# Kernel optimization log

Measured on AMD Instinct MI355X. Metric: run time of the kernel, lower is better.

The kernel has to match this reference:

```python
import jax, jax.numpy as jnp
import numpy as np

D_MODEL = 1024
NHEAD = 16
D_K = D_MODEL // NHEAD


def setup_inputs() -> dict:
    key = jax.random.key(0)
    ks = jax.random.split(key, 12)
    B, S = 1, 4096
    s = 1.0 / np.sqrt(D_MODEL)
    inp = {
        "query": jax.random.normal(ks[0], (B, S, D_MODEL), jnp.float32),
        "key": jax.random.normal(ks[1], (B, S, D_MODEL), jnp.float32),
        "value": jax.random.normal(ks[2], (B, S, D_MODEL), jnp.float32),
        "W_q": jax.random.normal(ks[3], (D_MODEL, D_MODEL), jnp.float32) * s,
        "b_q": jnp.zeros((D_MODEL,), jnp.float32),
        "W_k": jax.random.normal(ks[4], (D_MODEL, D_MODEL), jnp.float32) * s,
        "b_k": jnp.zeros((D_MODEL,), jnp.float32),
        "W_v": jax.random.normal(ks[5], (D_MODEL, D_MODEL), jnp.float32) * s,
        "b_v": jnp.zeros((D_MODEL,), jnp.float32),
        "W_o": jax.random.normal(ks[6], (D_MODEL, D_MODEL), jnp.float32) * s,
        "b_o": jnp.zeros((D_MODEL,), jnp.float32),
    }
    return inp


def reference(query, key, value, W_q, b_q, W_k, b_k, W_v, b_v, W_o, b_o):
    B, S, _ = query.shape
    # linear projections (torch Linear: x @ W.T + b)
    Q = query @ W_q.T + b_q
    K = key @ W_k.T + b_k
    V = value @ W_v.T + b_v
    # split heads: [B, S, D] -> [B, H, S, d_k]
    Q = Q.reshape(B, S, NHEAD, D_K).transpose(0, 2, 1, 3)
    K = K.reshape(B, S, NHEAD, D_K).transpose(0, 2, 1, 3)
    V = V.reshape(B, S, NHEAD, D_K).transpose(0, 2, 1, 3)
    # scaled dot-product attention (materializes [B,H,S,S] like original)
    scores = jnp.einsum("bhqd,bhkd->bhqk", Q, K) / jnp.sqrt(jnp.float32(D_K))
    weights = jax.nn.softmax(scores, axis=-1)
    attn = jnp.einsum("bhqk,bhkd->bhqd", weights, V)
    # combine heads: [B, H, S, d_k] -> [B, S, D]
    attn = attn.transpose(0, 2, 1, 3).reshape(B, S, D_MODEL)
    return attn @ W_o.T + b_o
```

## Files before the change

kernel.cpp:

```cpp
#include <hip/hip_runtime.h>
#include <hip/hip_bf16.h>
#include <type_traits>

constexpr int SEQ = 4096;
constexpr int DMODEL = 1024;
constexpr int NH = 16;
constexpr int DKH = 64;
constexpr float SCALE = 0.125f;
constexpr float SCALE2 = 0.125f * 1.4426950408889634f;

typedef __bf16 bf16x8 __attribute__((ext_vector_type(8)));
typedef __bf16 bf16x4 __attribute__((ext_vector_type(4)));
typedef float f32x4 __attribute__((ext_vector_type(4)));
typedef float f32x16 __attribute__((ext_vector_type(16)));
typedef unsigned int u32x4 __attribute__((ext_vector_type(4)));
union W8 { u32x4 u; bf16x8 v; };

__device__ inline void store_c(__hip_bfloat16* p, float v) { *p = __float2bfloat16(v); }
__device__ inline void store_c(float* p, float v) { *p = v; }

typedef const void __attribute__((address_space(1)))* gas_ptr;
typedef void __attribute__((address_space(3)))* las_ptr;
__device__ inline void load_lds_16B(const void* g, void* l) {
  __builtin_amdgcn_global_load_lds((gas_ptr)g, (las_ptr)l, 16, 0, 0);
}

__device__ inline unsigned pack2(float a, float b) {
  union { __bf16 h[2]; unsigned u; } p;
  p.h[0] = (__bf16)a; p.h[1] = (__bf16)b;
  return p.u;
}

__device__ inline void st8(__hip_bfloat16* buf, int row, int col, bf16x8 v) {
  *(bf16x8*)(buf + row * 64 + (col ^ ((row & 7) << 3))) = v;
}
__device__ inline bf16x8 ld8(const __hip_bfloat16* buf, int row, int col) {
  return *(const bf16x8*)(buf + row * 64 + (col ^ ((row & 7) << 3)));
}

__global__ __launch_bounds__(256)
void cvt_all(const float* __restrict__ q, const float* __restrict__ k,
             const float* __restrict__ v, const float* __restrict__ wq,
             const float* __restrict__ wk, const float* __restrict__ wv,
             const float* __restrict__ wo,
             __bf16* __restrict__ Xq, __bf16* __restrict__ Xk,
             __bf16* __restrict__ Xv, __bf16* __restrict__ Wqb,
             __bf16* __restrict__ Wkb, __bf16* __restrict__ Wvb,
             __bf16* __restrict__ Wob) {
  const int b = blockIdx.x;
  const float* src; __bf16* dst; size_t base;
  if      (b < 2048) { src = q;  dst = Xq;  base = b; }
  else if (b < 4096) { src = k;  dst = Xk;  base = b - 2048; }
  else if (b < 6144) { src = v;  dst = Xv;  base = b - 4096; }
  else if (b < 6656) { src = wq; dst = Wqb; base = b - 6144; }
  else if (b < 7168) { src = wk; dst = Wkb; base = b - 6656; }
  else if (b < 7680) { src = wv; dst = Wvb; base = b - 7168; }
  else               { src = wo; dst = Wob; base = b - 7680; }
  const size_t i = (base * 256 + threadIdx.x) * 8;
  const float4 a = *(const float4*)(src + i);
  const float4 c = *(const float4*)(src + i + 4);
  bf16x8 r = {(__bf16)a.x, (__bf16)a.y, (__bf16)a.z, (__bf16)a.w,
              (__bf16)c.x, (__bf16)c.y, (__bf16)c.z, (__bf16)c.w};
  *(bf16x8*)(dst + i) = r;
}

constexpr int BK = 64;

template <typename TC, bool TRANS_C>
__global__ __launch_bounds__(256)
void gemm_bf16_lds(const __bf16* __restrict__ A,
                   const __bf16* __restrict__ W,
                   const float* __restrict__ bias,
                   TC* __restrict__ C,
                   float out_scale) {
  __shared__ alignas(16) __bf16 As[64][64];
  __shared__ alignas(16) __bf16 Ws[64][64];

  const int t = threadIdx.x;
  const int lane = t & 63;
  const int w = t >> 6;
  const int wr = w >> 1;
  const int wc = w & 1;
  const int col = lane & 15;
  const int quad = lane >> 4;
  const int m_blk = blockIdx.y * 64;
  const int n_blk = blockIdx.x * 64;

  const int srow = t >> 3;
  const int scol = (t & 7) * 8;

  f32x4 acc[2][2] = {};

  for (int k0 = 0; k0 < DMODEL; k0 += BK) {
    __syncthreads();
    #pragma unroll
    for (int p = 0; p < 2; ++p)
      load_lds_16B(A + (size_t)(m_blk + p * 32 + srow) * DMODEL + k0 + scol,
                   &As[p * 32 + srow][scol]);
    #pragma unroll
    for (int p = 0; p < 2; ++p)
      load_lds_16B(W + (size_t)(n_blk + p * 32 + srow) * DMODEL + k0 + scol,
                   &Ws[p * 32 + srow][scol]);
    __syncthreads();

    #pragma unroll
    for (int kh = 0; kh < BK; kh += 32) {
      bf16x8 af[2], bfr[2];
      #pragma unroll
      for (int at = 0; at < 2; ++at)
        af[at] = *(const bf16x8*)&As[wr * 32 + at * 16 + col][kh + quad * 8];
      #pragma unroll
      for (int bt = 0; bt < 2; ++bt)
        bfr[bt] = *(const bf16x8*)&Ws[wc * 32 + bt * 16 + col][kh + quad * 8];
      #pragma unroll
      for (int at = 0; at < 2; ++at)
        #pragma unroll
        for (int bt = 0; bt < 2; ++bt)
          acc[at][bt] = __builtin_amdgcn_mfma_f32_16x16x32_bf16(
              af[at], bfr[bt], acc[at][bt], 0, 0, 0);
    }
  }

  #pragma unroll
  for (int at = 0; at < 2; ++at) {
    #pragma unroll
    for (int bt = 0; bt < 2; ++bt) {
      const int n = n_blk + wc * 32 + bt * 16 + col;
      const float b = bias[n];
      #pragma unroll
      for (int i = 0; i < 4; ++i) {
        const int m = m_blk + wr * 32 + at * 16 + quad * 4 + i;
        const float v = (acc[at][bt][i] + b) * out_scale;
        if constexpr (TRANS_C) store_c(&C[(size_t)n * SEQ + m], v);
        else                   store_c(&C[(size_t)m * DMODEL + n], v);
      }
    }
  }
}

constexpr int LDK = 72;

template <typename TA, typename TC, bool TRANS_C>
__global__ __launch_bounds__(256)
void gemm_tiled(const TA* __restrict__ A,
                const float* __restrict__ W,
                const float* __restrict__ bias,
                TC* __restrict__ C,
                float out_scale) {
  __shared__ alignas(16) __bf16 As[128][LDK];
  __shared__ alignas(16) __bf16 Ws[64][LDK];

  const int t = threadIdx.x;
  const int lane = t & 63;
  const int w = t >> 6;
  const int wr = w >> 1;
  const int wc = w & 1;
  const int col = lane & 15;
  const int quad = lane >> 4;
  const int m_blk = blockIdx.y * 128;
  const int n_blk = blockIdx.x * 64;

  f32x4 acc[4][2] = {};

  for (int k0 = 0; k0 < DMODEL; k0 += BK) {
    __syncthreads();
    if constexpr (std::is_same<TA, float>::value) {
      #pragma unroll
      for (int p = 0; p < 8; ++p) {
        const int r = p * 16 + (t >> 4);
        const int c = (t & 15) * 4;
        const float4 v =
            *(const float4*)(A + (size_t)(m_blk + r) * DMODEL + k0 + c);
        bf16x4 b = {(__bf16)v.x, (__bf16)v.y, (__bf16)v.z, (__bf16)v.w};
        *(bf16x4*)&As[r][c] = b;
      }
    } else {
      #pragma unroll
      for (int p = 0; p < 4; ++p) {
        const int r = p * 32 + (t >> 3);
        const int c = (t & 7) * 8;
        *(bf16x8*)&As[r][c] =
            *(const bf16x8*)((const __bf16*)A + (size_t)(m_blk + r) * DMODEL + k0 + c);
      }
    }
    #pragma unroll
    for (int p = 0; p < 4; ++p) {
      const int r = p * 16 + (t >> 4);
      const int c = (t & 15) * 4;
      const float4 v =
          *(const float4*)(W + (size_t)(n_blk + r) * DMODEL + k0 + c);
      bf16x4 b = {(__bf16)v.x, (__bf16)v.y, (__bf16)v.z, (__bf16)v.w};
      *(bf16x4*)&Ws[r][c] = b;
    }
    __syncthreads();

    #pragma unroll
    for (int kh = 0; kh < BK; kh += 32) {
      bf16x8 af[4], bfr[2];
      #pragma unroll
      for (int at = 0; at < 4; ++at)
        af[at] = *(const bf16x8*)&As[wr * 64 + at * 16 + col][kh + quad * 8];
      #pragma unroll
      for (int bt = 0; bt < 2; ++bt)
        bfr[bt] = *(const bf16x8*)&Ws[wc * 32 + bt * 16 + col][kh + quad * 8];
      #pragma unroll
      for (int at = 0; at < 4; ++at)
        #pragma unroll
        for (int bt = 0; bt < 2; ++bt)
          acc[at][bt] = __builtin_amdgcn_mfma_f32_16x16x32_bf16(
              af[at], bfr[bt], acc[at][bt], 0, 0, 0);
    }
  }

  #pragma unroll
  for (int at = 0; at < 4; ++at) {
    #pragma unroll
    for (int bt = 0; bt < 2; ++bt) {
      const int n = n_blk + wc * 32 + bt * 16 + col;
      const float b = bias[n];
      #pragma unroll
      for (int i = 0; i < 4; ++i) {
        const int m = m_blk + wr * 64 + at * 16 + quad * 4 + i;
        const float v = (acc[at][bt][i] + b) * out_scale;
        if constexpr (TRANS_C) store_c(&C[(size_t)n * SEQ + m], v);
        else                   store_c(&C[(size_t)m * DMODEL + n], v);
      }
    }
  }
}

__global__ __launch_bounds__(256, 4)
void flash_attn_split32(const __hip_bfloat16* __restrict__ Q,
                        const __hip_bfloat16* __restrict__ K,
                        const __hip_bfloat16* __restrict__ Vt,
                        __hip_bfloat16* __restrict__ Opart,
                        float* __restrict__ lsum_g) {
  __shared__ alignas(16) __hip_bfloat16 kt[64 * 64];
  __shared__ alignas(16) __hip_bfloat16 vtt[64 * 64];

  const int t = threadIdx.x;
  const int lane = t & 63;
  const int w = t >> 6;
  const int head = blockIdx.y;
  const int q0 = blockIdx.x * 128;
  const int z = blockIdx.z;
  const int l31 = lane & 31;
  const int hl = lane >> 5;

  bf16x8 qf[4];
  {
    const __hip_bfloat16* qp =
        Q + (size_t)(q0 + w * 32 + l31) * DMODEL + head * DKH + hl * 8;
    #pragma unroll
    for (int db = 0; db < 4; ++db) qf[db] = *(const bf16x8*)(qp + db * 16);
  }

  f32x16 acc_o[2] = {};
  float lsa = 0.f, lsb = 0.f;

  const int sr = t >> 2;
  const int sc = (t & 3) * 16;
  const int kbeg = z * (SEQ / 2);
  constexpr int NT = (SEQ / 2) / 64;

  const __hip_bfloat16* kgp = K + (size_t)(kbeg + sr) * DMODEL + head * DKH + sc;
  const __hip_bfloat16* vgp = Vt + (size_t)(head * DKH + sr) * SEQ + kbeg + sc;

  bf16x8 kr0 = *(const bf16x8*)kgp;
  bf16x8 kr1 = *(const bf16x8*)(kgp + 8);
  bf16x8 vr0 = *(const bf16x8*)vgp;
  bf16x8 vr1 = *(const bf16x8*)(vgp + 8);

  for (int ti = 0; ti < NT; ++ti) {
    __syncthreads();
    st8(kt, sr, sc, kr0);  st8(kt, sr, sc + 8, kr1);
    st8(vtt, sr, sc, vr0); st8(vtt, sr, sc + 8, vr1);
    __syncthreads();

    if (ti + 1 < NT) {
      const __hip_bfloat16* kn = kgp + (size_t)(ti + 1) * 64 * DMODEL;
      const __hip_bfloat16* vn = vgp + (ti + 1) * 64;
      kr0 = *(const bf16x8*)kn; kr1 = *(const bf16x8*)(kn + 8);
      vr0 = *(const bf16x8*)vn; vr1 = *(const bf16x8*)(vn + 8);
    }

    bf16x8 pa[4];
    #pragma unroll
    for (int kb = 0; kb < 2; ++kb) {
      f32x16 s = {};
      #pragma unroll
      for (int db = 0; db < 4; ++db) {
        const bf16x8 kf = ld8(kt, kb * 32 + l31, db * 16 + hl * 8);
        s = __builtin_amdgcn_mfma_f32_32x32x16_bf16(kf, qf[db], s, 0, 0, 0);
      }
      unsigned wp[8];
      #pragma unroll
      for (int i = 0; i < 8; ++i) {
        const float p0 = __builtin_amdgcn_exp2f(s[2 * i]);
        const float p1 = __builtin_amdgcn_exp2f(s[2 * i + 1]);
        lsa += p0; lsb += p1;
        wp[i] = pack2(p0, p1);
      }
      #pragma unroll
      for (int b = 0; b < 2; ++b) {
        const unsigned x0 = (unsigned)__shfl_xor((int)wp[4 * b + 0], 32);
        const unsigned x1 = (unsigned)__shfl_xor((int)wp[4 * b + 1], 32);
        const unsigned x2 = (unsigned)__shfl_xor((int)wp[4 * b + 2], 32);
        const unsigned x3 = (unsigned)__shfl_xor((int)wp[4 * b + 3], 32);
        W8 u;
        u.u[0] = hl ? x2 : wp[4 * b + 0];
        u.u[1] = hl ? x3 : wp[4 * b + 1];
        u.u[2] = hl ? wp[4 * b + 2] : x0;
        u.u[3] = hl ? wp[4 * b + 3] : x1;
        pa[kb * 2 + b] = u.v;
      }
    }

    #pragma unroll
    for (int db = 0; db < 2; ++db)
      #pragma unroll
      for (int kq = 0; kq < 4; ++kq) {
        const bf16x8 vb = ld8(vtt, db * 32 + l31, kq * 16 + hl * 8);
        acc_o[db] = __builtin_amdgcn_mfma_f32_32x32x16_bf16(
            pa[kq], vb, acc_o[db], 0, 0, 0);
      }
  }

  float lsumq = lsa + lsb;
  lsumq += __shfl_xor(lsumq, 32);
  if (lane < 32)
    lsum_g[((size_t)z * NH + head) * SEQ + q0 + w * 32 + lane] = lsumq;

  __hip_bfloat16* O = Opart + (size_t)z * SEQ * DMODEL;
  #pragma unroll
  for (int db = 0; db < 2; ++db)
    #pragma unroll
    for (int r = 0; r < 16; ++r) {
      const int qr = q0 + w * 32 + (r & 3) + 8 * (r >> 2) + 4 * hl;
      const int c = head * DKH + db * 32 + l31;
      O[(size_t)qr * DMODEL + c] = __float2bfloat16(acc_o[db][r]);
    }
}

__global__ __launch_bounds__(256)
void attn_combine(const __hip_bfloat16* __restrict__ Op,
                  const float* __restrict__ ls,
                  __hip_bfloat16* __restrict__ Ao) {
  const size_t i = ((size_t)blockIdx.x * 256 + threadIdx.x) * 8;
  const int qrow = (int)(i >> 10);
  const int h = (int)((i & 1023) >> 6);
  const float inv = 1.f / (ls[(size_t)h * SEQ + qrow] +
                           ls[(size_t)(NH + h) * SEQ + qrow]);
  const bf16x8 a = *(const bf16x8*)(Op + i);
  const bf16x8 b = *(const bf16x8*)(Op + (size_t)SEQ * DMODEL + i);
  bf16x8 r;
  #pragma unroll
  for (int j = 0; j < 8; ++j)
    r[j] = (__bf16)(((float)a[j] + (float)b[j]) * inv);
  *(bf16x8*)(Ao + i) = r;
}

constexpr int LDP = 72;
constexpr float SHIFT = 8.0f;

__global__ __launch_bounds__(256)
void flash_attn_mono(const __hip_bfloat16* __restrict__ Q,
                     const __hip_bfloat16* __restrict__ K,
                     const __hip_bfloat16* __restrict__ Vt,
                     __hip_bfloat16* __restrict__ O) {
  __shared__ alignas(16) __hip_bfloat16 kt[64][LDP];
  __shared__ alignas(16) __hip_bfloat16 vtt[DKH][LDP];
  __shared__ alignas(16) __hip_bfloat16 plT[4][32][LDP];

  const int t = threadIdx.x;
  const int lane = t & 63;
  const int w = t >> 6;
  const int h = blockIdx.y;
  const int q0 = blockIdx.x * 128;
  const int col = lane & 15;
  const int quad = lane >> 4;

  bf16x8 qf[2][2];
  #pragma unroll
  for (int rg = 0; rg < 2; ++rg) {
    const __hip_bfloat16* qptr =
        Q + (size_t)(q0 + w * 32 + rg * 16 + col) * DMODEL + h * DKH + quad * 8;
    qf[rg][0] = *(const bf16x8*)qptr;
    qf[rg][1] = *(const bf16x8*)(qptr + 32);
  }

  f32x4 acc_o[2][4] = {};
  float lsumq[2] = {0.f, 0.f};
  const int sr = t >> 2;
  const int sc = (t & 3) * 16;

  for (int k0 = 0; k0 < SEQ; k0 += 64) {
    __syncthreads();
    const __hip_bfloat16* kg = K + (size_t)(k0 + sr) * DMODEL + h * DKH + sc;
    *(bf16x8*)&kt[sr][sc]     = *(const bf16x8*)kg;
    *(bf16x8*)&kt[sr][sc + 8] = *(const bf16x8*)(kg + 8);
    const __hip_bfloat16* vg = Vt + (size_t)(h * DKH + sr) * SEQ + k0 + sc;
    *(bf16x8*)&vtt[sr][sc]     = *(const bf16x8*)vg;
    *(bf16x8*)&vtt[sr][sc + 8] = *(const bf16x8*)(vg + 8);
    __syncthreads();

    #pragma unroll
    for (int jt = 0; jt < 4; ++jt) {
      const bf16x8 kf0 = *(const bf16x8*)&kt[jt * 16 + col][quad * 8];
      const bf16x8 kf1 = *(const bf16x8*)&kt[jt * 16 + col][quad * 8 + 32];
      #pragma unroll
      for (int rg = 0; rg < 2; ++rg) {
        f32x4 zz = {0.f, 0.f, 0.f, 0.f};
        zz = __builtin_amdgcn_mfma_f32_16x16x32_bf16(kf0, qf[rg][0], zz, 0, 0, 0);
        zz = __builtin_amdgcn_mfma_f32_16x16x32_bf16(kf1, qf[rg][1], zz, 0, 0, 0);
        bf16x4 pk;
        #pragma unroll
        for (int r = 0; r < 4; ++r) {
          const float p = __expf(zz[r] - SHIFT);
          lsumq[rg] += p;
          pk[r] = (__bf16)p;
        }
        *(bf16x4*)&plT[w][rg * 16 + col][jt * 16 + quad * 4] = pk;
      }
    }

    bf16x8 pa[2][2];
    #pragma unroll
    for (int rg = 0; rg < 2; ++rg) {
      pa[rg][0] = *(const bf16x8*)&plT[w][rg * 16 + col][quad * 8];
      pa[rg][1] = *(const bf16x8*)&plT[w][rg * 16 + col][quad * 8 + 32];
    }
    #pragma unroll
    for (int jt = 0; jt < 4; ++jt) {
      const bf16x8 vb0 = *(const bf16x8*)&vtt[jt * 16 + col][quad * 8];
      const bf16x8 vb1 = *(const bf16x8*)&vtt[jt * 16 + col][quad * 8 + 32];
      #pragma unroll
      for (int rg = 0; rg < 2; ++rg) {
        acc_o[rg][jt] = __builtin_amdgcn_mfma_f32_16x16x32_bf16(
            pa[rg][0], vb0, acc_o[rg][jt], 0, 0, 0);
        acc_o[rg][jt] = __builtin_amdgcn_mfma_f32_16x16x32_bf16(
            pa[rg][1], vb1, acc_o[rg][jt], 0, 0, 0);
      }
    }
  }

  #pragma unroll
  for (int rg = 0; rg < 2; ++rg) {
    lsumq[rg] += __shfl_xor(lsumq[rg], 16);
    lsumq[rg] += __shfl_xor(lsumq[rg], 32);
  }
  float invr[2][4];
  #pragma unroll
  for (int rg = 0; rg < 2; ++rg)
    #pragma unroll
    for (int r = 0; r < 4; ++r)
      invr[rg][r] = 1.f / __shfl(lsumq[rg], quad * 4 + r);

  #pragma unroll
  for (int rg = 0; rg < 2; ++rg) {
    #pragma unroll
    for (int jt = 0; jt < 4; ++jt) {
      #pragma unroll
      for (int r = 0; r < 4; ++r) {
        const int qr = q0 + w * 32 + rg * 16 + quad * 4 + r;
        const int c = h * DKH + jt * 16 + col;
        O[(size_t)qr * DMODEL + c] = __float2bfloat16(acc_o[rg][jt][r] * invr[rg][r]);
      }
    }
  }
}

extern "C" void kernel_launch(void* const* d_in, const int* in_sizes, int n_in,
                              void* d_out, int out_size, void* d_ws, size_t ws_size,
                              hipStream_t stream) {
  const float* query = (const float*)d_in[0];
  const float* key   = (const float*)d_in[1];
  const float* value = (const float*)d_in[2];
  const float* W_q   = (const float*)d_in[3];
  const float* b_q   = (const float*)d_in[4];
  const float* W_k   = (const float*)d_in[5];
  const float* b_k   = (const float*)d_in[6];
  const float* W_v   = (const float*)d_in[7];
  const float* b_v   = (const float*)d_in[8];
  const float* W_o   = (const float*)d_in[9];
  const float* b_o   = (const float*)d_in[10];

  float* out = (float*)d_out;
  const size_t mat = (size_t)SEQ * DMODEL;
  const size_t MB = 1024 * 1024;

  char* ws = (char*)d_ws;
  __hip_bfloat16* Qp = (__hip_bfloat16*)d_out;
  __hip_bfloat16* Kp = (__hip_bfloat16*)ws;
  __hip_bfloat16* Vt = Kp + mat;

  dim3 gblock(256);
  dim3 ggrid(DMODEL / 64, SEQ / 64);

  if (ws_size >= 40 * MB) {
    __bf16* Xq  = (__bf16*)((char*)d_out + 8 * MB);
    __bf16* Xk  = (__bf16*)(ws + 16 * MB);
    __bf16* Xv  = (__bf16*)(ws + 24 * MB);
    __bf16* Wqb = (__bf16*)(ws + 32 * MB);
    __bf16* Wkb = (__bf16*)(ws + 34 * MB);
    __bf16* Wvb = (__bf16*)(ws + 36 * MB);
    __bf16* Wob = (__bf16*)(ws + 38 * MB);
    __hip_bfloat16* Opart = (__hip_bfloat16*)(ws + 16 * MB);
    float* lsum = (float*)(ws + 32 * MB);
    __hip_bfloat16* Ao = (__hip_bfloat16*)(ws + 16 * MB);

    hipLaunchKernelGGL(cvt_all, dim3(8192), gblock, 0, stream,
                       query, key, value, W_q, W_k, W_v, W_o,
                       Xq, Xk, Xv, Wqb, Wkb, Wvb, Wob);

    hipLaunchKernelGGL((gemm_bf16_lds<__hip_bfloat16, false>), ggrid, gblock,
                       0, stream, Xq, Wqb, b_q, Qp, SCALE2);
    hipLaunchKernelGGL((gemm_bf16_lds<__hip_bfloat16, false>), ggrid, gblock,
                       0, stream, Xk, Wkb, b_k, Kp, 1.0f);
    hipLaunchKernelGGL((gemm_bf16_lds<__hip_bfloat16, true>), ggrid, gblock,
                       0, stream, Xv, Wvb, b_v, Vt, 1.0f);

    dim3 agrid(SEQ / 128, NH, 2);
    hipLaunchKernelGGL(flash_attn_split32, agrid, gblock, 0, stream,
                       Qp, Kp, Vt, Opart, lsum);
    hipLaunchKernelGGL(attn_combine, dim3(2048), gblock, 0, stream,
                       Opart, lsum, Ao);

    hipLaunchKernelGGL((gemm_bf16_lds<float, false>), ggrid, gblock, 0, stream,
                       (const __bf16*)Ao, Wob, b_o, out, 1.0f);
  } else {
    __hip_bfloat16* Ao = Qp + mat;
    float* Cw = (float*)d_ws;
    dim3 fgrid(DMODEL / 64, SEQ / 128);
    hipLaunchKernelGGL((gemm_tiled<float, __hip_bfloat16, false>), fgrid, gblock,
                       0, stream, query, W_q, b_q, Qp, SCALE);
    hipLaunchKernelGGL((gemm_tiled<float, __hip_bfloat16, false>), fgrid, gblock,
                       0, stream, key, W_k, b_k, Kp, 1.0f);
    hipLaunchKernelGGL((gemm_tiled<float, __hip_bfloat16, true>), fgrid, gblock,
                       0, stream, value, W_v, b_v, Vt, 1.0f);
    dim3 agrid(SEQ / 128, NH);
    hipLaunchKernelGGL(flash_attn_mono, agrid, gblock, 0, stream, Qp, Kp, Vt, Ao);
    hipLaunchKernelGGL((gemm_tiled<__hip_bfloat16, float, false>), fgrid, gblock,
                       0, stream, Ao, W_o, b_o, Cw, 1.0f);
    hipMemcpyAsync(out, Cw, mat * sizeof(float), hipMemcpyDeviceToDevice, stream);
  }
}
```

Before: 293.6 us.

## Enlarge GEMM tiles to 128x64, batch QKV projections, tune attention inner loop

The bf16 GEMM now computes 128x64 output tiles per block, so each wave holds 4x2 MFMA accumulators and the A tile is reused across more columns. The three Q/K/V projections run as one launch with a z-dimension that selects the operands, which cuts launch count and fills the GPU with more blocks. In flash attention, the cross-half shuffles are replaced with v_permlane32_swap, and s_setprio raises wave priority around the MFMA sections. The cost is higher register and LDS use per block, which may lower occupancy.

```diff
diff --git a/kernel.cpp b/kernel.cpp
--- a/kernel.cpp
+++ b/kernel.cpp
@@ -68,12 +68,12 @@
 
 template <typename TC, bool TRANS_C>
 __global__ __launch_bounds__(256)
-void gemm_bf16_lds(const __bf16* __restrict__ A,
-                   const __bf16* __restrict__ W,
-                   const float* __restrict__ bias,
-                   TC* __restrict__ C,
-                   float out_scale) {
-  __shared__ alignas(16) __bf16 As[64][64];
+void gemm128(const __bf16* __restrict__ A,
+             const __bf16* __restrict__ W,
+             const float* __restrict__ bias,
+             TC* __restrict__ C,
+             float out_scale) {
+  __shared__ alignas(16) __bf16 As[128][64];
   __shared__ alignas(16) __bf16 Ws[64][64];
 
   const int t = threadIdx.x;
@@ -83,18 +83,18 @@
   const int wc = w & 1;
   const int col = lane & 15;
   const int quad = lane >> 4;
-  const int m_blk = blockIdx.y * 64;
+  const int m_blk = blockIdx.y * 128;
   const int n_blk = blockIdx.x * 64;
 
   const int srow = t >> 3;
   const int scol = (t & 7) * 8;
 
-  f32x4 acc[2][2] = {};
+  f32x4 acc[4][2] = {};
 
   for (int k0 = 0; k0 < DMODEL; k0 += BK) {
     __syncthreads();
     #pragma unroll
-    for (int p = 0; p < 2; ++p)
+    for (int p = 0; p < 4; ++p)
       load_lds_16B(A + (size_t)(m_blk + p * 32 + srow) * DMODEL + k0 + scol,
                    &As[p * 32 + srow][scol]);
     #pragma unroll
@@ -105,15 +105,15 @@
 
     #pragma unroll
     for (int kh = 0; kh < BK; kh += 32) {
-      bf16x8 af[2], bfr[2];
-      #pragma unroll
-      for (int at = 0; at < 2; ++at)
-        af[at] = *(const bf16x8*)&As[wr * 32 + at * 16 + col][kh + quad * 8];
+      bf16x8 af[4], bfr[2];
+      #pragma unroll
+      for (int at = 0; at < 4; ++at)
+        af[at] = *(const bf16x8*)&As[wr * 64 + at * 16 + col][kh + quad * 8];
       #pragma unroll
       for (int bt = 0; bt < 2; ++bt)
         bfr[bt] = *(const bf16x8*)&Ws[wc * 32 + bt * 16 + col][kh + quad * 8];
       #pragma unroll
-      for (int at = 0; at < 2; ++at)
+      for (int at = 0; at < 4; ++at)
         #pragma unroll
         for (int bt = 0; bt < 2; ++bt)
           acc[at][bt] = __builtin_amdgcn_mfma_f32_16x16x32_bf16(
@@ -122,17 +122,97 @@
   }
 
   #pragma unroll
-  for (int at = 0; at < 2; ++at) {
+  for (int at = 0; at < 4; ++at) {
     #pragma unroll
     for (int bt = 0; bt < 2; ++bt) {
       const int n = n_blk + wc * 32 + bt * 16 + col;
       const float b = bias[n];
       #pragma unroll
       for (int i = 0; i < 4; ++i) {
-        const int m = m_blk + wr * 32 + at * 16 + quad * 4 + i;
+        const int m = m_blk + wr * 64 + at * 16 + quad * 4 + i;
         const float v = (acc[at][bt][i] + b) * out_scale;
         if constexpr (TRANS_C) store_c(&C[(size_t)n * SEQ + m], v);
         else                   store_c(&C[(size_t)m * DMODEL + n], v);
+      }
+    }
+  }
+}
+
+__global__ __launch_bounds__(256)
+void gemm_qkv(const __bf16* __restrict__ Xq, const __bf16* __restrict__ Xk,
+              const __bf16* __restrict__ Xv, const __bf16* __restrict__ Wq,
+              const __bf16* __restrict__ Wk, const __bf16* __restrict__ Wv,
+              const float* __restrict__ bq, const float* __restrict__ bk,
+              const float* __restrict__ bv,
+              __hip_bfloat16* __restrict__ Cq, __hip_bfloat16* __restrict__ Ck,
+              __hip_bfloat16* __restrict__ Cv) {
+  __shared__ alignas(16) __bf16 As[128][64];
+  __shared__ alignas(16) __bf16 Ws[64][64];
+
+  const int z = blockIdx.z;
+  const __bf16* A = (z == 0) ? Xq : (z == 1) ? Xk : Xv;
+  const __bf16* W = (z == 0) ? Wq : (z == 1) ? Wk : Wv;
+  const float* bias = (z == 0) ? bq : (z == 1) ? bk : bv;
+  __hip_bfloat16* C = (z == 0) ? Cq : (z == 1) ? Ck : Cv;
+  const float out_scale = (z == 0) ? SCALE2 : 1.0f;
+
+  const int t = threadIdx.x;
+  const int lane = t & 63;
+  const int w = t >> 6;
+  const int wr = w >> 1;
+  const int wc = w & 1;
+  const int col = lane & 15;
+  const int quad = lane >> 4;
+  const int m_blk = blockIdx.y * 128;
+  const int n_blk = blockIdx.x * 64;
+
+  const int srow = t >> 3;
+  const int scol = (t & 7) * 8;
+
+  f32x4 acc[4][2] = {};
+
+  for (int k0 = 0; k0 < DMODEL; k0 += BK) {
+    __syncthreads();
+    #pragma unroll
+    for (int p = 0; p < 4; ++p)
+      load_lds_16B(A + (size_t)(m_blk + p * 32 + srow) * DMODEL + k0 + scol,
+                   &As[p * 32 + srow][scol]);
+    #pragma unroll
+    for (int p = 0; p < 2; ++p)
+      load_lds_16B(W + (size_t)(n_blk + p * 32 + srow) * DMODEL + k0 + scol,
+                   &Ws[p * 32 + srow][scol]);
+    __syncthreads();
+
+    #pragma unroll
+    for (int kh = 0; kh < BK; kh += 32) {
+      bf16x8 af[4], bfr[2];
+      #pragma unroll
+      for (int at = 0; at < 4; ++at)
+        af[at] = *(const bf16x8*)&As[wr * 64 + at * 16 + col][kh + quad * 8];
+      #pragma unroll
+      for (int bt = 0; bt < 2; ++bt)
+        bfr[bt] = *(const bf16x8*)&Ws[wc * 32 + bt * 16 + col][kh + quad * 8];
+      #pragma unroll
+      for (int at = 0; at < 4; ++at)
+        #pragma unroll
+        for (int bt = 0; bt < 2; ++bt)
+          acc[at][bt] = __builtin_amdgcn_mfma_f32_16x16x32_bf16(
+              af[at], bfr[bt], acc[at][bt], 0, 0, 0);
+    }
+  }
+
+  #pragma unroll
+  for (int at = 0; at < 4; ++at) {
+    #pragma unroll
+    for (int bt = 0; bt < 2; ++bt) {
+      const int n = n_blk + wc * 32 + bt * 16 + col;
+      const float b = bias[n];
+      #pragma unroll
+      for (int i = 0; i < 4; ++i) {
+        const int m = m_blk + wr * 64 + at * 16 + quad * 4 + i;
+        const float v = (acc[at][bt][i] + b) * out_scale;
+        if (z == 2) *(&C[(size_t)n * SEQ + m]) = __float2bfloat16(v);
+        else        *(&C[(size_t)m * DMODEL + n]) = __float2bfloat16(v);
       }
     }
   }
@@ -288,11 +368,13 @@
     #pragma unroll
     for (int kb = 0; kb < 2; ++kb) {
       f32x16 s = {};
+      __builtin_amdgcn_s_setprio(1);
       #pragma unroll
       for (int db = 0; db < 4; ++db) {
         const bf16x8 kf = ld8(kt, kb * 32 + l31, db * 16 + hl * 8);
         s = __builtin_amdgcn_mfma_f32_32x32x16_bf16(kf, qf[db], s, 0, 0, 0);
       }
+      __builtin_amdgcn_s_setprio(0);
       unsigned wp[8];
       #pragma unroll
       for (int i = 0; i < 8; ++i) {
@@ -303,19 +385,17 @@
       }
       #pragma unroll
       for (int b = 0; b < 2; ++b) {
-        const unsigned x0 = (unsigned)__shfl_xor((int)wp[4 * b + 0], 32);
-        const unsigned x1 = (unsigned)__shfl_xor((int)wp[4 * b + 1], 32);
-        const unsigned x2 = (unsigned)__shfl_xor((int)wp[4 * b + 2], 32);
-        const unsigned x3 = (unsigned)__shfl_xor((int)wp[4 * b + 3], 32);
+        unsigned a0 = wp[4 * b + 0], a2 = wp[4 * b + 2];
+        unsigned a1 = wp[4 * b + 1], a3 = wp[4 * b + 3];
+        asm("v_permlane32_swap_b32 %0, %1" : "+v"(a0), "+v"(a2));
+        asm("v_permlane32_swap_b32 %0, %1" : "+v"(a1), "+v"(a3));
         W8 u;
-        u.u[0] = hl ? x2 : wp[4 * b + 0];
-        u.u[1] = hl ? x3 : wp[4 * b + 1];
-        u.u[2] = hl ? wp[4 * b + 2] : x0;
-        u.u[3] = hl ? wp[4 * b + 3] : x1;
+        u.u[0] = a0; u.u[1] = a1; u.u[2] = a2; u.u[3] = a3;
         pa[kb * 2 + b] = u.v;
       }
     }
 
+    __builtin_amdgcn_s_setprio(1);
     #pragma unroll
     for (int db = 0; db < 2; ++db)
       #pragma unroll
@@ -324,6 +404,7 @@
         acc_o[db] = __builtin_amdgcn_mfma_f32_32x32x16_bf16(
             pa[kq], vb, acc_o[db], 0, 0, 0);
       }
+    __builtin_amdgcn_s_setprio(0);
   }
 
   float lsumq = lsa + lsb;
@@ -333,13 +414,14 @@
 
   __hip_bfloat16* O = Opart + (size_t)z * SEQ * DMODEL;
   #pragma unroll
-  for (int db = 0; db < 2; ++db)
+  for (int db = 0; db < 2; ++db) {
     #pragma unroll
     for (int r = 0; r < 16; ++r) {
       const int qr = q0 + w * 32 + (r & 3) + 8 * (r >> 2) + 4 * hl;
       const int c = head * DKH + db * 32 + l31;
       O[(size_t)qr * DMODEL + c] = __float2bfloat16(acc_o[db][r]);
     }
+  }
 }
 
 __global__ __launch_bounds__(256)
@@ -495,7 +577,6 @@
   __hip_bfloat16* Vt = Kp + mat;
 
   dim3 gblock(256);
-  dim3 ggrid(DMODEL / 64, SEQ / 64);
 
   if (ws_size >= 40 * MB) {
     __bf16* Xq  = (__bf16*)((char*)d_out + 8 * MB);
@@ -513,12 +594,10 @@
                        query, key, value, W_q, W_k, W_v, W_o,
                        Xq, Xk, Xv, Wqb, Wkb, Wvb, Wob);
 
-    hipLaunchKernelGGL((gemm_bf16_lds<__hip_bfloat16, false>), ggrid, gblock,
-                       0, stream, Xq, Wqb, b_q, Qp, SCALE2);
-    hipLaunchKernelGGL((gemm_bf16_lds<__hip_bfloat16, false>), ggrid, gblock,
-                       0, stream, Xk, Wkb, b_k, Kp, 1.0f);
-    hipLaunchKernelGGL((gemm_bf16_lds<__hip_bfloat16, true>), ggrid, gblock,
-                       0, stream, Xv, Wvb, b_v, Vt, 1.0f);
+    dim3 qkvgrid(DMODEL / 64, SEQ / 128, 3);
+    hipLaunchKernelGGL(gemm_qkv, qkvgrid, gblock, 0, stream,
+                       Xq, Xk, Xv, Wqb, Wkb, Wvb, b_q, b_k, b_v,
+                       Qp, Kp, Vt);
 
     dim3 agrid(SEQ / 128, NH, 2);
     hipLaunchKernelGGL(flash_attn_split32, agrid, gblock, 0, stream,
@@ -526,7 +605,8 @@
     hipLaunchKernelGGL(attn_combine, dim3(2048), gblock, 0, stream,
                        Opart, lsum, Ao);
 
-    hipLaunchKernelGGL((gemm_bf16_lds<float, false>), ggrid, gblock, 0, stream,
+    dim3 ogrid(DMODEL / 64, SEQ / 128);
+    hipLaunchKernelGGL((gemm128<float, false>), ogrid, gblock, 0, stream,
                        (const __bf16*)Ao, Wob, b_o, out, 1.0f);
   } else {
     __hip_bfloat16* Ao = Qp + mat;
```

Result: faster. 276.4 us (-5.9%).
